# Optimization experiments

Measured on AMD Instinct MI355X. Metric: run time of the kernel, lower is better.

The kernel has to match this reference:

```python
import jax, jax.numpy as jnp
import numpy as np

B, NQ, NK, QS, KS, H, VD = 16, 64, 512, 256, 256, 256, 256


def setup_inputs() -> dict:
    key = jax.random.key(0)
    k1, k2, k3, k4, k5, k6, k7 = jax.random.split(key, 7)
    return {
        "queries": jax.random.normal(k1, (B, NQ, QS), dtype=jnp.float32),
        "keys": jax.random.normal(k2, (B, NK, KS), dtype=jnp.float32),
        "values": jax.random.normal(k3, (B, NK, VD), dtype=jnp.float32),
        "valid_lens": jax.random.randint(k4, (B,), 1, NK + 1, dtype=jnp.int32),
        # learned params (nn.Linear with bias=False): W_q [QS,H], W_k [KS,H], w_v [H]
        "W_q": jax.random.normal(k5, (QS, H), dtype=jnp.float32) / np.sqrt(QS),
        "W_k": jax.random.normal(k6, (KS, H), dtype=jnp.float32) / np.sqrt(KS),
        "w_v": jax.random.normal(k7, (H,), dtype=jnp.float32) / np.sqrt(H),
    }


def reference(queries, keys, values, valid_lens, W_q, W_k, w_v):
    # project: q [B,nq,H], k [B,nk,H]
    q = jnp.einsum("bqd,dh->bqh", queries, W_q)
    k = jnp.einsum("bkd,dh->bkh", keys, W_k)
    # broadcast-add -> tanh -> score reduction via w_v: [B,nq,nk]
    features = jnp.tanh(q[:, :, None, :] + k[:, None, :, :])  # [B,nq,nk,H]
    scores = jnp.einsum("bqkh,h->bqk", features, w_v)
    # masked softmax over keys (positions >= valid_len masked out)
    mask = jnp.arange(scores.shape[-1])[None, None, :] < valid_lens[:, None, None]
    scores = jnp.where(mask, scores, -1e6)
    attn = jax.nn.softmax(scores, axis=-1)
    # weighted sum of values (dropout p=0 / eval mode => identity)
    return jnp.einsum("bqk,bkv->bqv", attn, values)
```

## Files before the change

### kernel.cpp

```cpp
#include <hip/hip_runtime.h>
#include <hip/hip_bf16.h>

#define BB 16
#define NQ 64
#define NK 512
#define HD 256

typedef __attribute__((ext_vector_type(8))) short short8;
typedef __attribute__((ext_vector_type(4))) float f32x4;

__device__ __forceinline__ ushort bf16_rne(float v) {
    unsigned u = __float_as_uint(v);
    return (ushort)((u + 0x7FFFu + ((u >> 16) & 1u)) >> 16);
}
__device__ __forceinline__ float bf16_to_f(ushort h) {
    return __uint_as_float(((unsigned)h) << 16);
}

__global__ __launch_bounds__(256, 2) void proj_fused2(
    const float* __restrict__ queries, const float* __restrict__ keys,
    const float* __restrict__ W_q, const float* __restrict__ W_k,
    float* __restrict__ qp, float* __restrict__ kp, float scale)
{
    __shared__ ushort AsH[64 * 64], AsL[64 * 64];
    __shared__ ushort BsH[64 * 64], BsL[64 * 64];

    const float* A; const float* W; float* C; int rows0;
    const int bx = blockIdx.x;
    if (bx < 16) { A = queries; W = W_q; C = qp; rows0 = bx * 64; }
    else         { A = keys;    W = W_k; C = kp; rows0 = (bx - 16) * 64; }
    const int cols0 = blockIdx.y * 64;

    const int t = threadIdx.x, lane = t & 63, wave = t >> 6;
    const int quad = lane >> 4, l15 = lane & 15;
    const int sr  = t >> 2;
    const int sc2 = (t & 3) * 2;

    f32x4 acc[4];
    #pragma unroll
    for (int j = 0; j < 4; ++j) acc[j] = (f32x4){0.f, 0.f, 0.f, 0.f};

    for (int k0 = 0; k0 < 256; k0 += 64) {
        const float* arow = &A[(size_t)(rows0 + sr) * 256 + k0 + sc2 * 8];
        float4 a0 = *(const float4*)&arow[0];
        float4 a1 = *(const float4*)&arow[4];
        float4 a2 = *(const float4*)&arow[8];
        float4 a3 = *(const float4*)&arow[12];
        float wvv[16];
        {
            const float* wsrc = &W[(size_t)(k0 + sc2 * 8) * 256 + cols0 + sr];
            #pragma unroll
            for (int e = 0; e < 16; ++e)
                wvv[e] = wsrc[(size_t)e * 256];
        }

        __syncthreads();

        float av[16] = {a0.x, a0.y, a0.z, a0.w, a1.x, a1.y, a1.z, a1.w,
                        a2.x, a2.y, a2.z, a2.w, a3.x, a3.y, a3.z, a3.w};
        short8 ah0, ah1, al0, al1, bh0, bh1, bl0, bl1;
        #pragma unroll
        for (int e = 0; e < 8; ++e) {
            ushort h0 = bf16_rne(av[e]);
            ushort h1 = bf16_rne(av[8 + e]);
            ah0[e] = (short)h0;
            ah1[e] = (short)h1;
            al0[e] = (short)bf16_rne(av[e] - bf16_to_f(h0));
            al1[e] = (short)bf16_rne(av[8 + e] - bf16_to_f(h1));
            ushort w0 = bf16_rne(wvv[e]);
            ushort w1 = bf16_rne(wvv[8 + e]);
            bh0[e] = (short)w0;
            bh1[e] = (short)w1;
            bl0[e] = (short)bf16_rne(wvv[e] - bf16_to_f(w0));
            bl1[e] = (short)bf16_rne(wvv[8 + e] - bf16_to_f(w1));
        }
        {
            int s0 = sr * 8 + ((sc2 + 0) ^ (sr & 7));
            int s1 = sr * 8 + ((sc2 + 1) ^ (sr & 7));
            *(short8*)&AsH[s0 * 8] = ah0;
            *(short8*)&AsH[s1 * 8] = ah1;
            *(short8*)&AsL[s0 * 8] = al0;
            *(short8*)&AsL[s1 * 8] = al1;
            *(short8*)&BsH[s0 * 8] = bh0;
            *(short8*)&BsH[s1 * 8] = bh1;
            *(short8*)&BsL[s0 * 8] = bl0;
            *(short8*)&BsL[s1 * 8] = bl1;
        }
        __syncthreads();

        #pragma unroll
        for (int ks = 0; ks < 2; ++ks) {
            const int c = ks * 4 + quad;
            short8 aH, aL, bH[4], bL[4];
            {
                int r = wave * 16 + l15;
                int slot = r * 8 + (c ^ (r & 7));
                aH = *(const short8*)&AsH[slot * 8];
                aL = *(const short8*)&AsL[slot * 8];
            }
            #pragma unroll
            for (int ns = 0; ns < 4; ++ns) {
                int n = ns * 16 + l15;
                int slot = n * 8 + (c ^ (n & 7));
                bH[ns] = *(const short8*)&BsH[slot * 8];
                bL[ns] = *(const short8*)&BsL[slot * 8];
            }
            #pragma unroll
            for (int ns = 0; ns < 4; ++ns)
                acc[ns] = __builtin_amdgcn_mfma_f32_16x16x32_bf16(aH, bH[ns], acc[ns], 0, 0, 0);
            #pragma unroll
            for (int ns = 0; ns < 4; ++ns)
                acc[ns] = __builtin_amdgcn_mfma_f32_16x16x32_bf16(aL, bH[ns], acc[ns], 0, 0, 0);
            #pragma unroll
            for (int ns = 0; ns < 4; ++ns)
                acc[ns] = __builtin_amdgcn_mfma_f32_16x16x32_bf16(aH, bL[ns], acc[ns], 0, 0, 0);
        }
    }

    const int rbase = rows0 + wave * 16 + quad * 4;
    #pragma unroll
    for (int ns = 0; ns < 4; ++ns) {
        int col = cols0 + ns * 16 + l15;
        #pragma unroll
        for (int r = 0; r < 4; ++r)
            C[(size_t)(rbase + r) * 256 + col] =
                __builtin_amdgcn_exp2f(acc[ns][r] * scale);
    }
}

__global__ __launch_bounds__(256, 4) void score_a2(
    const float* __restrict__ qp,
    const float* __restrict__ kp,
    const int*   __restrict__ vlens,
    const float* __restrict__ w_v,
    float* __restrict__ Pt)
{
    __shared__ float eq[8][260];
    __shared__ float wv[HD];

    const int b   = blockIdx.x & 15;
    const int qt  = blockIdx.x >> 4;
    const int seg = blockIdx.y;
    const int vl  = vlens[b];

    const int t = threadIdx.x, lane = t & 63, wave = t >> 6;
    const int key = wave * 16 + (lane >> 2);
    const int ch  = lane & 3;
    const int kg  = seg * 64 + key;

    if (seg * 64 >= vl) {
        if (ch == 0) {
            float* dst = &Pt[((size_t)b * NK + kg) * 64 + qt * 8];
            *(float4*)&dst[0] = make_float4(0.f, 0.f, 0.f, 0.f);
            *(float4*)&dst[4] = make_float4(0.f, 0.f, 0.f, 0.f);
        }
        return;
    }

    const float* krow = kp + ((size_t)b * NK + kg) * HD + ch * 4;
    float4 ek[16];
    #pragma unroll
    for (int j = 0; j < 16; ++j) ek[j] = *(const float4*)&krow[j * 16];

    const float* qsrc = qp + ((size_t)b * NQ + qt * 8) * HD;
    #pragma unroll
    for (int i = 0; i < 2; ++i) {
        int idx = i * 256 + t;
        int row = idx >> 6, c4 = (idx & 63) * 4;
        *(float4*)&eq[row][c4] = *(const float4*)&qsrc[(size_t)row * HD + c4];
    }
    if (t < 64) *(float4*)&wv[t * 4] = *(const float4*)&w_v[t * 4];
    __syncthreads();

    float Wsum;
    {
        float ws = wv[lane] + wv[lane + 64] + wv[lane + 128] + wv[lane + 192];
        #pragma unroll
        for (int off = 32; off; off >>= 1) ws += __shfl_xor(ws, off);
        Wsum = ws;
    }

    float s[8] = {0.f, 0.f, 0.f, 0.f, 0.f, 0.f, 0.f, 0.f};
    #pragma unroll
    for (int j = 0; j < 16; ++j) {
        const int h = j * 16 + ch * 4;
        float4 e4 = ek[j];
        float4 w4 = *(const float4*)&wv[h];
        #pragma unroll
        for (int qi = 0; qi < 8; ++qi) {
            float4 q4 = *(const float4*)&eq[qi][h];
            float p0 = fmaf(q4.x, e4.x, 1.f);
            float p1 = fmaf(q4.y, e4.y, 1.f);
            float p2 = fmaf(q4.z, e4.z, 1.f);
            float p3 = fmaf(q4.w, e4.w, 1.f);
            float d01 = p0 * p1;
            float d23 = p2 * p3;
            float n01 = fmaf(w4.x, p1, w4.y * p0);
            float n23 = fmaf(w4.z, p3, w4.w * p2);
            float num = fmaf(d01, n23, d23 * n01);
            float r   = __builtin_amdgcn_rcpf(d01 * d23);
            s[qi] = fmaf(num, r, s[qi]);
        }
    }
    #pragma unroll
    for (int qi = 0; qi < 8; ++qi) {
        s[qi] += __shfl_xor(s[qi], 1);
        s[qi] += __shfl_xor(s[qi], 2);
    }

    if (ch == 0) {
        const bool masked = (kg >= vl);
        const float L2E = 1.4426950408889634f;
        float pt[8];
        #pragma unroll
        for (int qi = 0; qi < 8; ++qi) {
            float sv = fmaf(-2.f, s[qi], Wsum);
            pt[qi] = masked ? 0.f : __builtin_amdgcn_exp2f(sv * L2E);
        }
        float* dst = &Pt[((size_t)b * NK + kg) * 64 + qt * 8];
        *(float4*)&dst[0] = make_float4(pt[0], pt[1], pt[2], pt[3]);
        *(float4*)&dst[4] = make_float4(pt[4], pt[5], pt[6], pt[7]);
    }
}

__global__ __launch_bounds__(512) void pv_c(
    const float* __restrict__ Pt,
    const float* __restrict__ values,
    float* __restrict__ out)
{
    __shared__ f32x4 red[3][8][64];
    __shared__ float Lred[4][8];

    const int bx  = blockIdx.x;
    const int b   = bx & 15;
    const int qt  = (bx >> 4) & 7;
    const int vdq = bx >> 7;

    const int t   = threadIdx.x;
    const int vd4 = t & 15;
    const int q   = (t >> 4) & 7;
    const int kp4 = t >> 7;

    const float* vptr = values + (size_t)b * NK * HD + vdq * 64 + vd4 * 4;
    const float* pptr = Pt + (size_t)b * NK * 64 + qt * 8 + q;

    f32x4 acc = (f32x4){0.f, 0.f, 0.f, 0.f};
    float Lacc = 0.f;
    #pragma unroll 8
    for (int i = 0; i < NK / 4; ++i) {
        const int k = kp4 + 4 * i;
        float  p = pptr[(size_t)k * 64];
        float4 v = *(const float4*)&vptr[(size_t)k * HD];
        acc[0] = fmaf(p, v.x, acc[0]);
        acc[1] = fmaf(p, v.y, acc[1]);
        acc[2] = fmaf(p, v.z, acc[2]);
        acc[3] = fmaf(p, v.w, acc[3]);
        Lacc += p;
    }

    if (kp4 > 0) {
        red[kp4 - 1][q][vd4] = acc;
        if (vd4 == 0) Lred[kp4][q] = Lacc;
    }
    __syncthreads();
    if (kp4 == 0) {
        #pragma unroll
        for (int j = 0; j < 3; ++j) {
            f32x4 o = red[j][q][vd4];
            acc[0] += o[0]; acc[1] += o[1]; acc[2] += o[2]; acc[3] += o[3];
        }
        float L = Lacc + Lred[1][q] + Lred[2][q] + Lred[3][q];
        float r = __builtin_amdgcn_rcpf(L);
        float4 o = make_float4(acc[0] * r, acc[1] * r, acc[2] * r, acc[3] * r);
        *(float4*)&out[((size_t)(b * 64 + qt * 8 + q)) * 256 + vdq * 64 + vd4 * 4] = o;
    }
}

extern "C" void kernel_launch(void* const* d_in, const int* in_sizes, int n_in,
                              void* d_out, int out_size, void* d_ws, size_t ws_size,
                              hipStream_t stream) {
    const float* queries = (const float*)d_in[0];
    const float* keys    = (const float*)d_in[1];
    const float* values  = (const float*)d_in[2];
    const int*   vlens   = (const int*)d_in[3];
    const float* W_q     = (const float*)d_in[4];
    const float* W_k     = (const float*)d_in[5];
    const float* w_v     = (const float*)d_in[6];
    float* out = (float*)d_out;

    float* kp = (float*)d_ws;
    float* qp = kp + (size_t)BB * NK * HD;
    float* Pt = qp + (size_t)BB * NQ * HD;

    const float SC = 2.885390081777927f;

    proj_fused2<<<dim3(144, 4), 256, 0, stream>>>(queries, keys, W_q, W_k,
                                                  qp, kp, SC);
    score_a2<<<dim3(128, 8), 256, 0, stream>>>(qp, kp, vlens, w_v, Pt);
    pv_c<<<dim3(512), 512, 0, stream>>>(Pt, values, out);
}
```

Measured before the change: 125.3 us.

## Fuse projection, score and PV kernels into one cooperative persistent kernel

Merges the three kernels into a single cooperative launch of 512 blocks, with grid-wide syncs between the projection, score and PV phases. Shared memory is unioned across the phases. Each block loops over projection tiles, takes two score tasks, and does the PV work with 256 threads instead of 512. This removes two kernel launch gaps. In exchange it adds grid-sync costs, puts a 576-tile projection onto 512 blocks (two rounds for some), and lowers PV parallelism per block.

```diff
diff --git a/kernel.cpp b/kernel.cpp
--- a/kernel.cpp
+++ b/kernel.cpp
@@ -1,5 +1,8 @@
 #include <hip/hip_runtime.h>
+#include <hip/hip_cooperative_groups.h>
 #include <hip/hip_bf16.h>
+
+namespace cg = cooperative_groups;
 
 #define BB 16
 #define NQ 64
@@ -17,262 +20,259 @@
     return __uint_as_float(((unsigned)h) << 16);
 }
 
-__global__ __launch_bounds__(256, 2) void proj_fused2(
+__global__ __launch_bounds__(256, 2) void fused_all(
     const float* __restrict__ queries, const float* __restrict__ keys,
-    const float* __restrict__ W_q, const float* __restrict__ W_k,
-    float* __restrict__ qp, float* __restrict__ kp, float scale)
+    const float* __restrict__ values,  const int* __restrict__ vlens,
+    const float* __restrict__ W_q,     const float* __restrict__ W_k,
+    const float* __restrict__ w_v,
+    float* __restrict__ qp, float* __restrict__ kp,
+    float* __restrict__ Pt, float* __restrict__ out, float scale)
 {
-    __shared__ ushort AsH[64 * 64], AsL[64 * 64];
-    __shared__ ushort BsH[64 * 64], BsL[64 * 64];
-
-    const float* A; const float* W; float* C; int rows0;
-    const int bx = blockIdx.x;
-    if (bx < 16) { A = queries; W = W_q; C = qp; rows0 = bx * 64; }
-    else         { A = keys;    W = W_k; C = kp; rows0 = (bx - 16) * 64; }
-    const int cols0 = blockIdx.y * 64;
-
+    __shared__ __align__(16) union {
+        struct { ushort AsH[4096], AsL[4096], BsH[4096], BsL[4096]; } p;
+        struct { float eq[8][260]; float wv[HD]; } s;
+        struct { f32x4 red[128]; float Lred[8]; } v;
+    } u;
+
+    const int bid = blockIdx.x;
     const int t = threadIdx.x, lane = t & 63, wave = t >> 6;
-    const int quad = lane >> 4, l15 = lane & 15;
-    const int sr  = t >> 2;
-    const int sc2 = (t & 3) * 2;
-
-    f32x4 acc[4];
-    #pragma unroll
-    for (int j = 0; j < 4; ++j) acc[j] = (f32x4){0.f, 0.f, 0.f, 0.f};
-
-    for (int k0 = 0; k0 < 256; k0 += 64) {
-        const float* arow = &A[(size_t)(rows0 + sr) * 256 + k0 + sc2 * 8];
-        float4 a0 = *(const float4*)&arow[0];
-        float4 a1 = *(const float4*)&arow[4];
-        float4 a2 = *(const float4*)&arow[8];
-        float4 a3 = *(const float4*)&arow[12];
-        float wvv[16];
+    cg::grid_group grid = cg::this_grid();
+
+    for (int tile = bid; tile < 576; tile += 512) {
+        const int bx = tile % 144;
+        const int cols0 = (tile / 144) * 64;
+        const float* A; const float* W; float* C; int rows0;
+        if (bx < 16) { A = queries; W = W_q; C = qp; rows0 = bx * 64; }
+        else         { A = keys;    W = W_k; C = kp; rows0 = (bx - 16) * 64; }
+
+        const int quad = lane >> 4, l15 = lane & 15;
+        const int sr  = t >> 2;
+        const int sc2 = (t & 3) * 2;
+
+        f32x4 acc[4];
+        #pragma unroll
+        for (int j = 0; j < 4; ++j) acc[j] = (f32x4){0.f, 0.f, 0.f, 0.f};
+
+        for (int k0 = 0; k0 < 256; k0 += 64) {
+            const float* arow = &A[(size_t)(rows0 + sr) * 256 + k0 + sc2 * 8];
+            float4 a0 = *(const float4*)&arow[0];
+            float4 a1 = *(const float4*)&arow[4];
+            float4 a2 = *(const float4*)&arow[8];
+            float4 a3 = *(const float4*)&arow[12];
+            float wvv[16];
+            {
+                const float* wsrc = &W[(size_t)(k0 + sc2 * 8) * 256 + cols0 + sr];
+                #pragma unroll
+                for (int e = 0; e < 16; ++e)
+                    wvv[e] = wsrc[(size_t)e * 256];
+            }
+
+            __syncthreads();
+
+            float av[16] = {a0.x, a0.y, a0.z, a0.w, a1.x, a1.y, a1.z, a1.w,
+                            a2.x, a2.y, a2.z, a2.w, a3.x, a3.y, a3.z, a3.w};
+            short8 ah0, ah1, al0, al1, bh0, bh1, bl0, bl1;
+            #pragma unroll
+            for (int e = 0; e < 8; ++e) {
+                ushort h0 = bf16_rne(av[e]);
+                ushort h1 = bf16_rne(av[8 + e]);
+                ah0[e] = (short)h0;
+                ah1[e] = (short)h1;
+                al0[e] = (short)bf16_rne(av[e] - bf16_to_f(h0));
+                al1[e] = (short)bf16_rne(av[8 + e] - bf16_to_f(h1));
+                ushort w0 = bf16_rne(wvv[e]);
+                ushort w1 = bf16_rne(wvv[8 + e]);
+                bh0[e] = (short)w0;
+                bh1[e] = (short)w1;
+                bl0[e] = (short)bf16_rne(wvv[e] - bf16_to_f(w0));
+                bl1[e] = (short)bf16_rne(wvv[8 + e] - bf16_to_f(w1));
+            }
+            {
+                int s0 = sr * 8 + ((sc2 + 0) ^ (sr & 7));
+                int s1 = sr * 8 + ((sc2 + 1) ^ (sr & 7));
+                *(short8*)&u.p.AsH[s0 * 8] = ah0;
+                *(short8*)&u.p.AsH[s1 * 8] = ah1;
+                *(short8*)&u.p.AsL[s0 * 8] = al0;
+                *(short8*)&u.p.AsL[s1 * 8] = al1;
+                *(short8*)&u.p.BsH[s0 * 8] = bh0;
+                *(short8*)&u.p.BsH[s1 * 8] = bh1;
+                *(short8*)&u.p.BsL[s0 * 8] = bl0;
+                *(short8*)&u.p.BsL[s1 * 8] = bl1;
+            }
+            __syncthreads();
+
+            #pragma unroll
+            for (int ks = 0; ks < 2; ++ks) {
+                const int c = ks * 4 + quad;
+                short8 aH, aL, bH[4], bL[4];
+                {
+                    int r = wave * 16 + l15;
+                    int slot = r * 8 + (c ^ (r & 7));
+                    aH = *(const short8*)&u.p.AsH[slot * 8];
+                    aL = *(const short8*)&u.p.AsL[slot * 8];
+                }
+                #pragma unroll
+                for (int ns = 0; ns < 4; ++ns) {
+                    int n = ns * 16 + l15;
+                    int slot = n * 8 + (c ^ (n & 7));
+                    bH[ns] = *(const short8*)&u.p.BsH[slot * 8];
+                    bL[ns] = *(const short8*)&u.p.BsL[slot * 8];
+                }
+                #pragma unroll
+                for (int ns = 0; ns < 4; ++ns)
+                    acc[ns] = __builtin_amdgcn_mfma_f32_16x16x32_bf16(aH, bH[ns], acc[ns], 0, 0, 0);
+                #pragma unroll
+                for (int ns = 0; ns < 4; ++ns)
+                    acc[ns] = __builtin_amdgcn_mfma_f32_16x16x32_bf16(aL, bH[ns], acc[ns], 0, 0, 0);
+                #pragma unroll
+                for (int ns = 0; ns < 4; ++ns)
+                    acc[ns] = __builtin_amdgcn_mfma_f32_16x16x32_bf16(aH, bL[ns], acc[ns], 0, 0, 0);
+            }
+        }
+
+        const int rbase = rows0 + wave * 16 + quad * 4;
+        #pragma unroll
+        for (int ns = 0; ns < 4; ++ns) {
+            int col = cols0 + ns * 16 + l15;
+            #pragma unroll
+            for (int r = 0; r < 4; ++r)
+                C[(size_t)(rbase + r) * 256 + col] =
+                    __builtin_amdgcn_exp2f(acc[ns][r] * scale);
+        }
+    }
+
+    grid.sync();
+
+    for (int r = 0; r < 2; ++r) {
+        const int task = bid * 2 + r;
+        const int b   = task & 15;
+        const int qt  = (task >> 4) & 7;
+        const int seg = task >> 7;
+        const int vl  = vlens[b];
+
+        const int key = wave * 16 + (lane >> 2);
+        const int ch  = lane & 3;
+        const int kg  = seg * 64 + key;
+
+        if (seg * 64 >= vl) {
+            if (ch == 0) {
+                float* dst = &Pt[((size_t)b * NK + kg) * 64 + qt * 8];
+                *(float4*)&dst[0] = make_float4(0.f, 0.f, 0.f, 0.f);
+                *(float4*)&dst[4] = make_float4(0.f, 0.f, 0.f, 0.f);
+            }
+            continue;
+        }
+
+        const float* krow = kp + ((size_t)b * NK + kg) * HD + ch * 4;
+        float4 ek[16];
+        #pragma unroll
+        for (int j = 0; j < 16; ++j) ek[j] = *(const float4*)&krow[j * 16];
+
+        const float* qsrc = qp + ((size_t)b * NQ + qt * 8) * HD;
+        #pragma unroll
+        for (int i = 0; i < 2; ++i) {
+            int idx = i * 256 + t;
+            int row = idx >> 6, c4 = (idx & 63) * 4;
+            *(float4*)&u.s.eq[row][c4] = *(const float4*)&qsrc[(size_t)row * HD + c4];
+        }
+        if (t < 64) *(float4*)&u.s.wv[t * 4] = *(const float4*)&w_v[t * 4];
+        __syncthreads();
+
+        float Wsum;
         {
-            const float* wsrc = &W[(size_t)(k0 + sc2 * 8) * 256 + cols0 + sr];
-            #pragma unroll
-            for (int e = 0; e < 16; ++e)
-                wvv[e] = wsrc[(size_t)e * 256];
-        }
-
+            float ws = u.s.wv[lane] + u.s.wv[lane + 64] +
+                       u.s.wv[lane + 128] + u.s.wv[lane + 192];
+            #pragma unroll
+            for (int off = 32; off; off >>= 1) ws += __shfl_xor(ws, off);
+            Wsum = ws;
+        }
+
+        float s[8] = {0.f, 0.f, 0.f, 0.f, 0.f, 0.f, 0.f, 0.f};
+        #pragma unroll
+        for (int j = 0; j < 16; ++j) {
+            const int h = j * 16 + ch * 4;
+            float4 e4 = ek[j];
+            float4 w4 = *(const float4*)&u.s.wv[h];
+            #pragma unroll
+            for (int qi = 0; qi < 8; ++qi) {
+                float4 q4 = *(const float4*)&u.s.eq[qi][h];
+                float p0 = fmaf(q4.x, e4.x, 1.f);
+                float p1 = fmaf(q4.y, e4.y, 1.f);
+                float p2 = fmaf(q4.z, e4.z, 1.f);
+                float p3 = fmaf(q4.w, e4.w, 1.f);
+                float d01 = p0 * p1;
+                float d23 = p2 * p3;
+                float n01 = fmaf(w4.x, p1, w4.y * p0);
+                float n23 = fmaf(w4.z, p3, w4.w * p2);
+                float num = fmaf(d01, n23, d23 * n01);
+                float rr  = __builtin_amdgcn_rcpf(d01 * d23);
+                s[qi] = fmaf(num, rr, s[qi]);
+            }
+        }
+        #pragma unroll
+        for (int qi = 0; qi < 8; ++qi) {
+            s[qi] += __shfl_xor(s[qi], 1);
+            s[qi] += __shfl_xor(s[qi], 2);
+        }
+
+        if (ch == 0) {
+            const bool masked = (kg >= vl);
+            const float L2E = 1.4426950408889634f;
+            float pt[8];
+            #pragma unroll
+            for (int qi = 0; qi < 8; ++qi) {
+                float sv = fmaf(-2.f, s[qi], Wsum);
+                pt[qi] = masked ? 0.f : __builtin_amdgcn_exp2f(sv * L2E);
+            }
+            float* dst = &Pt[((size_t)b * NK + kg) * 64 + qt * 8];
+            *(float4*)&dst[0] = make_float4(pt[0], pt[1], pt[2], pt[3]);
+            *(float4*)&dst[4] = make_float4(pt[4], pt[5], pt[6], pt[7]);
+        }
         __syncthreads();
-
-        float av[16] = {a0.x, a0.y, a0.z, a0.w, a1.x, a1.y, a1.z, a1.w,
-                        a2.x, a2.y, a2.z, a2.w, a3.x, a3.y, a3.z, a3.w};
-        short8 ah0, ah1, al0, al1, bh0, bh1, bl0, bl1;
-        #pragma unroll
-        for (int e = 0; e < 8; ++e) {
-            ushort h0 = bf16_rne(av[e]);
-            ushort h1 = bf16_rne(av[8 + e]);
-            ah0[e] = (short)h0;
-            ah1[e] = (short)h1;
-            al0[e] = (short)bf16_rne(av[e] - bf16_to_f(h0));
-            al1[e] = (short)bf16_rne(av[8 + e] - bf16_to_f(h1));
-            ushort w0 = bf16_rne(wvv[e]);
-            ushort w1 = bf16_rne(wvv[8 + e]);
-            bh0[e] = (short)w0;
-            bh1[e] = (short)w1;
-            bl0[e] = (short)bf16_rne(wvv[e] - bf16_to_f(w0));
-            bl1[e] = (short)bf16_rne(wvv[8 + e] - bf16_to_f(w1));
-        }
-        {
-            int s0 = sr * 8 + ((sc2 + 0) ^ (sr & 7));
-            int s1 = sr * 8 + ((sc2 + 1) ^ (sr & 7));
-            *(short8*)&AsH[s0 * 8] = ah0;
-            *(short8*)&AsH[s1 * 8] = ah1;
-            *(short8*)&AsL[s0 * 8] = al0;
-            *(short8*)&AsL[s1 * 8] = al1;
-            *(short8*)&BsH[s0 * 8] = bh0;
-            *(short8*)&BsH[s1 * 8] = bh1;
-            *(short8*)&BsL[s0 * 8] = bl0;
-            *(short8*)&BsL[s1 * 8] = bl1;
+    }
+
+    grid.sync();
+
+    {
+        const int b   = bid & 15;
+        const int qt  = (bid >> 4) & 7;
+        const int vdq = bid >> 7;
+
+        const int vd4 = t & 15;
+        const int q   = (t >> 4) & 7;
+        const int kp2 = t >> 7;
+
+        const float* vptr = values + (size_t)b * NK * HD + vdq * 64 + vd4 * 4;
+        const float* pptr = Pt + (size_t)b * NK * 64 + qt * 8 + q;
+
+        f32x4 acc = (f32x4){0.f, 0.f, 0.f, 0.f};
+        float Lacc = 0.f;
+        #pragma unroll 16
+        for (int i = 0; i < NK / 2; ++i) {
+            const int k = kp2 + 2 * i;
+            float  p = pptr[(size_t)k * 64];
+            float4 v = *(const float4*)&vptr[(size_t)k * HD];
+            acc[0] = fmaf(p, v.x, acc[0]);
+            acc[1] = fmaf(p, v.y, acc[1]);
+            acc[2] = fmaf(p, v.z, acc[2]);
+            acc[3] = fmaf(p, v.w, acc[3]);
+            Lacc += p;
+        }
+
+        if (kp2 == 1) {
+            u.v.red[t - 128] = acc;
+            if (vd4 == 0) u.v.Lred[q] = Lacc;
         }
         __syncthreads();
-
-        #pragma unroll
-        for (int ks = 0; ks < 2; ++ks) {
-            const int c = ks * 4 + quad;
-            short8 aH, aL, bH[4], bL[4];
-            {
-                int r = wave * 16 + l15;
-                int slot = r * 8 + (c ^ (r & 7));
-                aH = *(const short8*)&AsH[slot * 8];
-                aL = *(const short8*)&AsL[slot * 8];
-            }
-            #pragma unroll
-            for (int ns = 0; ns < 4; ++ns) {
-                int n = ns * 16 + l15;
-                int slot = n * 8 + (c ^ (n & 7));
-                bH[ns] = *(const short8*)&BsH[slot * 8];
-                bL[ns] = *(const short8*)&BsL[slot * 8];
-            }
-            #pragma unroll
-            for (int ns = 0; ns < 4; ++ns)
-                acc[ns] = __builtin_amdgcn_mfma_f32_16x16x32_bf16(aH, bH[ns], acc[ns], 0, 0, 0);
-            #pragma unroll
-            for (int ns = 0; ns < 4; ++ns)
-                acc[ns] = __builtin_amdgcn_mfma_f32_16x16x32_bf16(aL, bH[ns], acc[ns], 0, 0, 0);
-            #pragma unroll
-            for (int ns = 0; ns < 4; ++ns)
-                acc[ns] = __builtin_amdgcn_mfma_f32_16x16x32_bf16(aH, bL[ns], acc[ns], 0, 0, 0);
-        }
-    }
-
-    const int rbase = rows0 + wave * 16 + quad * 4;
-    #pragma unroll
-    for (int ns = 0; ns < 4; ++ns) {
-        int col = cols0 + ns * 16 + l15;
-        #pragma unroll
-        for (int r = 0; r < 4; ++r)
-            C[(size_t)(rbase + r) * 256 + col] =
-                __builtin_amdgcn_exp2f(acc[ns][r] * scale);
-    }
-}
-
-__global__ __launch_bounds__(256, 4) void score_a2(
-    const float* __restrict__ qp,
-    const float* __restrict__ kp,
-    const int*   __restrict__ vlens,
-    const float* __restrict__ w_v,
-    float* __restrict__ Pt)
-{
-    __shared__ float eq[8][260];
-    __shared__ float wv[HD];
-
-    const int b   = blockIdx.x & 15;
-    const int qt  = blockIdx.x >> 4;
-    const int seg = blockIdx.y;
-    const int vl  = vlens[b];
-
-    const int t = threadIdx.x, lane = t & 63, wave = t >> 6;
-    const int key = wave * 16 + (lane >> 2);
-    const int ch  = lane & 3;
-    const int kg  = seg * 64 + key;
-
-    if (seg * 64 >= vl) {
-        if (ch == 0) {
-            float* dst = &Pt[((size_t)b * NK + kg) * 64 + qt * 8];
-            *(float4*)&dst[0] = make_float4(0.f, 0.f, 0.f, 0.f);
-            *(float4*)&dst[4] = make_float4(0.f, 0.f, 0.f, 0.f);
-        }
-        return;
-    }
-
-    const float* krow = kp + ((size_t)b * NK + kg) * HD + ch * 4;
-    float4 ek[16];
-    #pragma unroll
-    for (int j = 0; j < 16; ++j) ek[j] = *(const float4*)&krow[j * 16];
-
-    const float* qsrc = qp + ((size_t)b * NQ + qt * 8) * HD;
-    #pragma unroll
-    for (int i = 0; i < 2; ++i) {
-        int idx = i * 256 + t;
-        int row = idx >> 6, c4 = (idx & 63) * 4;
-        *(float4*)&eq[row][c4] = *(const float4*)&qsrc[(size_t)row * HD + c4];
-    }
-    if (t < 64) *(float4*)&wv[t * 4] = *(const float4*)&w_v[t * 4];
-    __syncthreads();
-
-    float Wsum;
-    {
-        float ws = wv[lane] + wv[lane + 64] + wv[lane + 128] + wv[lane + 192];
-        #pragma unroll
-        for (int off = 32; off; off >>= 1) ws += __shfl_xor(ws, off);
-        Wsum = ws;
-    }
-
-    float s[8] = {0.f, 0.f, 0.f, 0.f, 0.f, 0.f, 0.f, 0.f};
-    #pragma unroll
-    for (int j = 0; j < 16; ++j) {
-        const int h = j * 16 + ch * 4;
-        float4 e4 = ek[j];
-        float4 w4 = *(const float4*)&wv[h];
-        #pragma unroll
-        for (int qi = 0; qi < 8; ++qi) {
-            float4 q4 = *(const float4*)&eq[qi][h];
-            float p0 = fmaf(q4.x, e4.x, 1.f);
-            float p1 = fmaf(q4.y, e4.y, 1.f);
-            float p2 = fmaf(q4.z, e4.z, 1.f);
-            float p3 = fmaf(q4.w, e4.w, 1.f);
-            float d01 = p0 * p1;
-            float d23 = p2 * p3;
-            float n01 = fmaf(w4.x, p1, w4.y * p0);
-            float n23 = fmaf(w4.z, p3, w4.w * p2);
-            float num = fmaf(d01, n23, d23 * n01);
-            float r   = __builtin_amdgcn_rcpf(d01 * d23);
-            s[qi] = fmaf(num, r, s[qi]);
-        }
-    }
-    #pragma unroll
-    for (int qi = 0; qi < 8; ++qi) {
-        s[qi] += __shfl_xor(s[qi], 1);
-        s[qi] += __shfl_xor(s[qi], 2);
-    }
-
-    if (ch == 0) {
-        const bool masked = (kg >= vl);
-        const float L2E = 1.4426950408889634f;
-        float pt[8];
-        #pragma unroll
-        for (int qi = 0; qi < 8; ++qi) {
-            float sv = fmaf(-2.f, s[qi], Wsum);
-            pt[qi] = masked ? 0.f : __builtin_amdgcn_exp2f(sv * L2E);
-        }
-        float* dst = &Pt[((size_t)b * NK + kg) * 64 + qt * 8];
-        *(float4*)&dst[0] = make_float4(pt[0], pt[1], pt[2], pt[3]);
-        *(float4*)&dst[4] = make_float4(pt[4], pt[5], pt[6], pt[7]);
-    }
-}
-
-__global__ __launch_bounds__(512) void pv_c(
-    const float* __restrict__ Pt,
-    const float* __restrict__ values,
-    float* __restrict__ out)
-{
-    __shared__ f32x4 red[3][8][64];
-    __shared__ float Lred[4][8];
-
-    const int bx  = blockIdx.x;
-    const int b   = bx & 15;
-    const int qt  = (bx >> 4) & 7;
-    const int vdq = bx >> 7;
-
-    const int t   = threadIdx.x;
-    const int vd4 = t & 15;
-    const int q   = (t >> 4) & 7;
-    const int kp4 = t >> 7;
-
-    const float* vptr = values + (size_t)b * NK * HD + vdq * 64 + vd4 * 4;
-    const float* pptr = Pt + (size_t)b * NK * 64 + qt * 8 + q;
-
-    f32x4 acc = (f32x4){0.f, 0.f, 0.f, 0.f};
-    float Lacc = 0.f;
-    #pragma unroll 8
-    for (int i = 0; i < NK / 4; ++i) {
-        const int k = kp4 + 4 * i;
-        float  p = pptr[(size_t)k * 64];
-        float4 v = *(const float4*)&vptr[(size_t)k * HD];
-        acc[0] = fmaf(p, v.x, acc[0]);
-        acc[1] = fmaf(p, v.y, acc[1]);
-        acc[2] = fmaf(p, v.z, acc[2]);
-        acc[3] = fmaf(p, v.w, acc[3]);
-        Lacc += p;
-    }
-
-    if (kp4 > 0) {
-        red[kp4 - 1][q][vd4] = acc;
-        if (vd4 == 0) Lred[kp4][q] = Lacc;
-    }
-    __syncthreads();
-    if (kp4 == 0) {
-        #pragma unroll
-        for (int j = 0; j < 3; ++j) {
-            f32x4 o = red[j][q][vd4];
+        if (kp2 == 0) {
+            f32x4 o = u.v.red[t];
             acc[0] += o[0]; acc[1] += o[1]; acc[2] += o[2]; acc[3] += o[3];
-        }
-        float L = Lacc + Lred[1][q] + Lred[2][q] + Lred[3][q];
-        float r = __builtin_amdgcn_rcpf(L);
-        float4 o = make_float4(acc[0] * r, acc[1] * r, acc[2] * r, acc[3] * r);
-        *(float4*)&out[((size_t)(b * 64 + qt * 8 + q)) * 256 + vdq * 64 + vd4 * 4] = o;
+            float L = Lacc + u.v.Lred[q];
+            float rr = __builtin_amdgcn_rcpf(L);
+            float4 ov = make_float4(acc[0] * rr, acc[1] * rr,
+                                    acc[2] * rr, acc[3] * rr);
+            *(float4*)&out[((size_t)(b * 64 + qt * 8 + q)) * 256 + vdq * 64 + vd4 * 4] = ov;
+        }
     }
 }
 
@@ -292,10 +292,13 @@
     float* qp = kp + (size_t)BB * NK * HD;
     float* Pt = qp + (size_t)BB * NQ * HD;
 
-    const float SC = 2.885390081777927f;
-
-    proj_fused2<<<dim3(144, 4), 256, 0, stream>>>(queries, keys, W_q, W_k,
-                                                  qp, kp, SC);
-    score_a2<<<dim3(128, 8), 256, 0, stream>>>(qp, kp, vlens, w_v, Pt);
-    pv_c<<<dim3(512), 512, 0, stream>>>(Pt, values, out);
+    float SC = 2.885390081777927f;
+
+    void* args[] = {
+        (void*)&queries, (void*)&keys, (void*)&values, (void*)&vlens,
+        (void*)&W_q, (void*)&W_k, (void*)&w_v,
+        (void*)&qp, (void*)&kp, (void*)&Pt, (void*)&out, (void*)&SC,
+    };
+    hipLaunchCooperativeKernel((void*)fused_all, dim3(512), dim3(256),
+                               args, 0, stream);
 }
```

After: 264.0 us. +110.6%, slower.
